# Kernel optimization log

Measured on AMD Instinct MI355X. Metric: run time of the kernel, lower is better.

Reference implementation:

```python
import jax, jax.numpy as jnp
import numpy as np

HID = 5120
H_DEV = 16          # 128 heads / 8 devices
NOPE = 128
ROPE = 64
VDIM = 128
QH = NOPE + ROPE    # 192
Q_LORA = 1536
KV_LORA = 512
EPS = 1e-6
SCALE_DEV = 1.0 / 8.0
ROPE_BASE = 10000.0


def rmsnorm(x, w):
    var = jnp.mean(x * x, axis=-1, keepdims=True)
    return x * jax.lax.rsqrt(var + EPS) * w


def apply_rope(x, pos):
    # DeepSeek-V2: interleaved->blocked reorder, then rotate-half RoPE.
    d = x.shape[-1]
    x = jnp.concatenate([x[..., 0::2], x[..., 1::2]], axis=-1)
    inv = 1.0 / (ROPE_BASE ** (jnp.arange(0, d, 2, dtype=jnp.float32) / d))  # [d/2]
    ang = pos[:, None, :, None].astype(jnp.float32) * inv                     # [b,1,s,d/2]
    cos = jnp.concatenate([jnp.cos(ang), jnp.cos(ang)], axis=-1)
    sin = jnp.concatenate([jnp.sin(ang), jnp.sin(ang)], axis=-1)
    x1, x2 = x[..., : d // 2], x[..., d // 2:]
    return x * cos + jnp.concatenate([-x2, x1], axis=-1) * sin


def setup_inputs() -> dict:
    key = jax.random.key(0)
    ks = jax.random.split(key, 16)
    b, s, past = 1, 2048, 2048
    w = lambda k, shape: (jax.random.normal(k, shape, jnp.float32) * 0.02)
    return {
        "hidden_states": jax.random.normal(ks[0], (b, s, HID), jnp.float32),
        "position_ids": jnp.arange(b * s, dtype=jnp.int32).reshape(b, s),
        "attention_mask": jnp.zeros((b, 1, s, past + s), jnp.float32),
        "past_k": jax.random.normal(ks[1], (b, H_DEV, past, QH), jnp.float32),
        "past_v": jax.random.normal(ks[2], (b, H_DEV, past, VDIM), jnp.float32),
        "w_in_ln": jnp.ones((HID,), jnp.float32),
        "w_qa": w(ks[3], (Q_LORA, HID)),
        "w_qa_ln": jnp.ones((Q_LORA,), jnp.float32),
        "w_qb": w(ks[4], (H_DEV * QH, Q_LORA)),
        "w_kva": w(ks[5], (KV_LORA + ROPE, HID)),
        "w_kva_ln": jnp.ones((KV_LORA,), jnp.float32),
        "w_kvb": w(ks[6], (H_DEV * (NOPE + VDIM), KV_LORA)),
        "w_o": w(ks[7], (HID, H_DEV * VDIM)),
    }


def reference(hidden_states, position_ids, attention_mask, past_k, past_v,
              w_in_ln, w_qa, w_qa_ln, w_qb, w_kva, w_kva_ln, w_kvb, w_o):
    b, s, _ = hidden_states.shape
    residual = hidden_states * SCALE_DEV
    x = rmsnorm(hidden_states, w_in_ln)

    # MLA query: low-rank down, RMSNorm, up to per-device heads
    q = rmsnorm(x @ w_qa.T, w_qa_ln) @ w_qb.T                       # [b,s,H*QH]
    q = q.reshape(b, s, H_DEV, QH).transpose(0, 2, 1, 3)            # [b,H,s,QH]
    q_nope, q_pe = q[..., :NOPE], q[..., NOPE:]

    # MLA key/value: joint compressed kv + shared rope key
    ckv = x @ w_kva.T                                                # [b,s,KV_LORA+ROPE]
    c_kv, k_pe = ckv[..., :KV_LORA], ckv[..., KV_LORA:]
    kv = rmsnorm(c_kv, w_kva_ln) @ w_kvb.T                           # [b,s,H*(NOPE+V)]
    kv = kv.reshape(b, s, H_DEV, NOPE + VDIM).transpose(0, 2, 1, 3)  # [b,H,s,NOPE+V]
    k_nope, v = kv[..., :NOPE], kv[..., NOPE:]
    k_pe = k_pe.reshape(b, 1, s, ROPE)

    q_pe = apply_rope(q_pe, position_ids)
    k_pe = apply_rope(k_pe, position_ids)

    q = jnp.concatenate([q_nope, q_pe], axis=-1)                     # [b,H,s,QH]
    k = jnp.concatenate([k_nope, jnp.broadcast_to(k_pe, (b, H_DEV, s, ROPE))], axis=-1)

    # KV-cache concat -> present kv
    k = jnp.concatenate([past_k, k], axis=2)                         # [b,H,s_kv,QH]
    v = jnp.concatenate([past_v, v], axis=2)                         # [b,H,s_kv,V]

    scores = jnp.einsum('bhqd,bhkd->bhqk', q, k) * (QH ** -0.5) + attention_mask
    attn = jax.nn.softmax(scores, axis=-1)
    ctx = jnp.einsum('bhqk,bhkd->bhqd', attn, v)                     # [b,H,s,V]
    ctx = ctx.transpose(0, 2, 1, 3).reshape(b, s, H_DEV * VDIM)

    out = residual + ctx @ w_o.T
    return out.astype(jnp.float32), k.astype(jnp.float32), v.astype(jnp.float32)
```

## Files before the change

### kernel.cpp

```cpp
#include <hip/hip_runtime.h>
#include <cstdint>

typedef unsigned short ushort_t;
typedef __attribute__((ext_vector_type(8))) short short8;
typedef __attribute__((ext_vector_type(4))) float floatx4;

#define HID    5120
#define NHEAD  16
#define NOPE   128
#define ROPE_D 64
#define VDIM   128
#define QHD    192
#define QLORA  1536
#define KVLORA 512
#define SEQ    2048
#define PAST   2048
#define TOTK   4096
#define NQAKV  2112
#define EPS_RMS 1e-6f
#define SCALE_DEV 0.125f
#define LOG2E 1.4426950408889634f
#define ATT_SCALE 0.07216878364870322f
#define LOG2_10000 13.287712379549449f

__device__ __forceinline__ float bf2f(ushort_t u) {
  unsigned int x = ((unsigned int)u) << 16;
  return __builtin_bit_cast(float, x);
}
__device__ __forceinline__ ushort_t f2bf(float f) {
  unsigned int u = __builtin_bit_cast(unsigned int, f);
  unsigned int r = u + 0x7fffu + ((u >> 16) & 1u);
  return (ushort_t)(r >> 16);
}
__device__ __forceinline__ void unpack8(uint4 c, float* f) {
  const ushort_t* p = (const ushort_t*)&c;
#pragma unroll
  for (int i = 0; i < 8; ++i) f[i] = bf2f(p[i]);
}
__device__ __forceinline__ uint4 pack8(const float* f) {
  uint4 c;
  ushort_t* p = (ushort_t*)&c;
#pragma unroll
  for (int i = 0; i < 8; ++i) p[i] = f2bf(f[i]);
  return c;
}

__global__ void cvt_kernel(const float* __restrict__ src, ushort_t* __restrict__ dst)
{
  long i = ((long)blockIdx.x * 256 + threadIdx.x) * 8;
  float f[8];
  *(float4*)(f)     = *(const float4*)(src + i);
  *(float4*)(f + 4) = *(const float4*)(src + i + 4);
  *(uint4*)(dst + i) = pack8(f);
}

__global__ void zero4_kernel(uint4* __restrict__ dst)
{
  long i = (long)blockIdx.x * 256 + threadIdx.x;
  uint4 z; z.x = 0u; z.y = 0u; z.z = 0u; z.w = 0u;
  dst[i] = z;
}

#define GLDT 40
__global__ __launch_bounds__(256, 2) void gemm_bt(
    const ushort_t* __restrict__ A, const ushort_t* __restrict__ B,
    ushort_t* __restrict__ Cb, float* __restrict__ Cf,
    const float* __restrict__ resid, float resid_scale,
    int M, int N, int K)
{
  __shared__ __align__(16) ushort_t As[128 * GLDT];
  __shared__ __align__(16) ushort_t Bs[128 * GLDT];
  int t = threadIdx.x;
  int lane = t & 63, wave = t >> 6;
  int wm = wave >> 1, wn = wave & 1;
  int lrow = lane & 15, quad = lane >> 4;
  long bm = (long)blockIdx.y * 128;
  long bn = (long)blockIdx.x * 128;

  int r0 = t >> 2, cc = t & 3;
  int r1 = r0 + 64;
  const ushort_t* a0 = A + (bm + r0) * (long)K + cc * 8;
  const ushort_t* a1 = A + (bm + r1) * (long)K + cc * 8;
  long nb0 = bn + r0; if (nb0 > N - 1) nb0 = N - 1;
  long nb1 = bn + r1; if (nb1 > N - 1) nb1 = N - 1;
  const ushort_t* b0 = B + nb0 * (long)K + cc * 8;
  const ushort_t* b1 = B + nb1 * (long)K + cc * 8;

  floatx4 acc[4][4];
#pragma unroll
  for (int i = 0; i < 4; ++i)
#pragma unroll
    for (int j = 0; j < 4; ++j) acc[i][j] = (floatx4)0.f;

  uint4 pa0 = *(const uint4*)a0;
  uint4 pa1 = *(const uint4*)a1;
  uint4 pb0 = *(const uint4*)b0;
  uint4 pb1 = *(const uint4*)b1;

  int nk = K >> 5;
  for (int kt = 0; kt < nk; ++kt) {
    *(uint4*)&As[r0 * GLDT + cc * 8] = pa0;
    *(uint4*)&As[r1 * GLDT + cc * 8] = pa1;
    *(uint4*)&Bs[r0 * GLDT + cc * 8] = pb0;
    *(uint4*)&Bs[r1 * GLDT + cc * 8] = pb1;
    __syncthreads();
    if (kt + 1 < nk) {
      int off = (kt + 1) << 5;
      pa0 = *(const uint4*)(a0 + off);
      pa1 = *(const uint4*)(a1 + off);
      pb0 = *(const uint4*)(b0 + off);
      pb1 = *(const uint4*)(b1 + off);
    }
    short8 af[4], bfr[4];
#pragma unroll
    for (int mt = 0; mt < 4; ++mt)
      af[mt] = *(const short8*)&As[(wm * 64 + mt * 16 + lrow) * GLDT + quad * 8];
#pragma unroll
    for (int nt = 0; nt < 4; ++nt)
      bfr[nt] = *(const short8*)&Bs[(wn * 64 + nt * 16 + lrow) * GLDT + quad * 8];
#pragma unroll
    for (int mt = 0; mt < 4; ++mt)
#pragma unroll
      for (int nt = 0; nt < 4; ++nt)
        acc[mt][nt] = __builtin_amdgcn_mfma_f32_16x16x32_bf16(af[mt], bfr[nt], acc[mt][nt], 0, 0, 0);
    __syncthreads();
  }

#pragma unroll
  for (int mt = 0; mt < 4; ++mt) {
    long grow = bm + wm * 64 + mt * 16 + quad * 4;
#pragma unroll
    for (int nt = 0; nt < 4; ++nt) {
      long gcol = bn + wn * 64 + nt * 16 + lrow;
      if (gcol < N) {
#pragma unroll
        for (int r2 = 0; r2 < 4; ++r2) {
          long row = grow + r2;
          float v = acc[mt][nt][r2];
          if (Cf) {
            if (resid) v += resid_scale * resid[row * (long)N + gcol];
            Cf[row * (long)N + gcol] = v;
          } else {
            Cb[row * (long)N + gcol] = f2bf(v);
          }
        }
      }
    }
  }
}

__global__ __launch_bounds__(256, 2) void gemm_splitk(
    const ushort_t* __restrict__ A, const ushort_t* __restrict__ B,
    float* __restrict__ Cf, int M, int N, int K)
{
  __shared__ __align__(16) ushort_t As[128 * GLDT];
  __shared__ __align__(16) ushort_t Bs[128 * GLDT];
  int t = threadIdx.x;
  int lane = t & 63, wave = t >> 6;
  int wm = wave >> 1, wn = wave & 1;
  int lrow = lane & 15, quad = lane >> 4;
  long bm = (long)blockIdx.y * 128;
  long bn = (long)blockIdx.x * 128;
  int khalf = K >> 1;
  long k0 = (long)blockIdx.z * khalf;

  int r0 = t >> 2, cc = t & 3;
  int r1 = r0 + 64;
  const ushort_t* a0 = A + (bm + r0) * (long)K + k0 + cc * 8;
  const ushort_t* a1 = A + (bm + r1) * (long)K + k0 + cc * 8;
  long nb0 = bn + r0; if (nb0 > N - 1) nb0 = N - 1;
  long nb1 = bn + r1; if (nb1 > N - 1) nb1 = N - 1;
  const ushort_t* b0 = B + nb0 * (long)K + k0 + cc * 8;
  const ushort_t* b1 = B + nb1 * (long)K + k0 + cc * 8;

  floatx4 acc[4][4];
#pragma unroll
  for (int i = 0; i < 4; ++i)
#pragma unroll
    for (int j = 0; j < 4; ++j) acc[i][j] = (floatx4)0.f;

  uint4 pa0 = *(const uint4*)a0;
  uint4 pa1 = *(const uint4*)a1;
  uint4 pb0 = *(const uint4*)b0;
  uint4 pb1 = *(const uint4*)b1;

  int nk = khalf >> 5;
  for (int kt = 0; kt < nk; ++kt) {
    *(uint4*)&As[r0 * GLDT + cc * 8] = pa0;
    *(uint4*)&As[r1 * GLDT + cc * 8] = pa1;
    *(uint4*)&Bs[r0 * GLDT + cc * 8] = pb0;
    *(uint4*)&Bs[r1 * GLDT + cc * 8] = pb1;
    __syncthreads();
    if (kt + 1 < nk) {
      int off = (kt + 1) << 5;
      pa0 = *(const uint4*)(a0 + off);
      pa1 = *(const uint4*)(a1 + off);
      pb0 = *(const uint4*)(b0 + off);
      pb1 = *(const uint4*)(b1 + off);
    }
    short8 af[4], bfr[4];
#pragma unroll
    for (int mt = 0; mt < 4; ++mt)
      af[mt] = *(const short8*)&As[(wm * 64 + mt * 16 + lrow) * GLDT + quad * 8];
#pragma unroll
    for (int nt = 0; nt < 4; ++nt)
      bfr[nt] = *(const short8*)&Bs[(wn * 64 + nt * 16 + lrow) * GLDT + quad * 8];
#pragma unroll
    for (int mt = 0; mt < 4; ++mt)
#pragma unroll
      for (int nt = 0; nt < 4; ++nt)
        acc[mt][nt] = __builtin_amdgcn_mfma_f32_16x16x32_bf16(af[mt], bfr[nt], acc[mt][nt], 0, 0, 0);
    __syncthreads();
  }

#pragma unroll
  for (int mt = 0; mt < 4; ++mt) {
    long grow = bm + wm * 64 + mt * 16 + quad * 4;
#pragma unroll
    for (int nt = 0; nt < 4; ++nt) {
      long gcol = bn + wn * 64 + nt * 16 + lrow;
      if (gcol < N) {
#pragma unroll
        for (int r2 = 0; r2 < 4; ++r2)
          atomicAdd(&Cf[(grow + r2) * (long)N + gcol], acc[mt][nt][r2]);
      }
    }
  }
}

__global__ void rms_in_kernel(const float* __restrict__ x,
                              const float* __restrict__ w,
                              ushort_t* __restrict__ out)
{
  int row = blockIdx.x, t = threadIdx.x;
  const float* xr = x + (long)row * HID + t * 16;
  float v[16];
#pragma unroll
  for (int i = 0; i < 4; ++i) *(float4*)(v + i * 4) = *(const float4*)(xr + i * 4);
  float ss = 0.f;
#pragma unroll
  for (int i = 0; i < 16; ++i) ss += v[i] * v[i];
#pragma unroll
  for (int o = 1; o < 64; o <<= 1) ss += __shfl_xor(ss, o);
  __shared__ float red[5];
  if ((t & 63) == 0) red[t >> 6] = ss;
  __syncthreads();
  float tot = red[0] + red[1] + red[2] + red[3] + red[4];
  float sc = rsqrtf(tot / (float)HID + EPS_RMS);
  float wv[16];
#pragma unroll
  for (int i = 0; i < 4; ++i) *(float4*)(wv + i * 4) = *(const float4*)(w + t * 16 + i * 4);
#pragma unroll
  for (int i = 0; i < 16; ++i) v[i] *= sc * wv[i];
  ushort_t* o = out + (long)row * HID + t * 16;
  *(uint4*)o       = pack8(v);
  *(uint4*)(o + 8) = pack8(v + 8);
}

__global__ void rms_qa_f32(const float* __restrict__ C,
                           const float* __restrict__ w,
                           ushort_t* __restrict__ out)
{
  int row = blockIdx.x, t = threadIdx.x;
  const float* xr = C + (long)row * NQAKV + t * 8;
  float v[8];
  *(float4*)(v)     = *(const float4*)(xr);
  *(float4*)(v + 4) = *(const float4*)(xr + 4);
  float ss = 0.f;
#pragma unroll
  for (int i = 0; i < 8; ++i) ss += v[i] * v[i];
#pragma unroll
  for (int o = 1; o < 64; o <<= 1) ss += __shfl_xor(ss, o);
  __shared__ float red[3];
  if ((t & 63) == 0) red[t >> 6] = ss;
  __syncthreads();
  float tot = red[0] + red[1] + red[2];
  float sc = rsqrtf(tot / (float)QLORA + EPS_RMS);
  float wv[8];
  *(float4*)(wv)     = *(const float4*)(w + t * 8);
  *(float4*)(wv + 4) = *(const float4*)(w + t * 8 + 4);
#pragma unroll
  for (int i = 0; i < 8; ++i) v[i] *= sc * wv[i];
  *(uint4*)(out + (long)row * QLORA + t * 8) = pack8(v);
}

__global__ void rms_ckv_rope_f32(const float* __restrict__ C,
                                 const float* __restrict__ w,
                                 const int* __restrict__ pos_ids,
                                 ushort_t* __restrict__ ckv_n,
                                 ushort_t* __restrict__ kpe,
                                 float* __restrict__ k_out)
{
  int row = blockIdx.x, t = threadIdx.x;
  const float* xr = C + (long)row * NQAKV + QLORA;
  float v[8];
  *(float4*)(v)     = *(const float4*)(xr + t * 8);
  *(float4*)(v + 4) = *(const float4*)(xr + t * 8 + 4);
  float ss = 0.f;
#pragma unroll
  for (int i = 0; i < 8; ++i) ss += v[i] * v[i];
#pragma unroll
  for (int o = 1; o < 64; o <<= 1) ss += __shfl_xor(ss, o);
  float sc = rsqrtf(ss / (float)KVLORA + EPS_RMS);
  float wv[8];
  *(float4*)(wv)     = *(const float4*)(w + t * 8);
  *(float4*)(wv + 4) = *(const float4*)(w + t * 8 + 4);
  float ov[8];
#pragma unroll
  for (int i = 0; i < 8; ++i) ov[i] = v[i] * sc * wv[i];
  *(uint4*)(ckv_n + (long)row * KVLORA + t * 8) = pack8(ov);

  if (t < 32) {
    float e  = xr[512 + 2 * t];
    float od = xr[512 + 2 * t + 1];
    float p = (float)pos_ids[row];
    float inv = __builtin_exp2f(-((float)t / 32.f) * LOG2_10000);
    float ang = p * inv, sn, cs;
    sincosf(ang, &sn, &cs);
    float r1 = e * cs - od * sn;
    float r2 = od * cs + e * sn;
    kpe[(long)row * 64 + t]      = f2bf(r1);
    kpe[(long)row * 64 + 32 + t] = f2bf(r2);
#pragma unroll
    for (int h = 0; h < NHEAD; ++h) {
      float* kr = k_out + ((long)h * TOTK + PAST + row) * QHD + NOPE;
      kr[t] = r1;
      kr[32 + t] = r2;
    }
  }
}

__global__ void qpost_kernel(const ushort_t* __restrict__ q_raw,
                             const int* __restrict__ pos_ids,
                             ushort_t* __restrict__ q_bf)
{
  int row = blockIdx.x, t = threadIdx.x;
  const ushort_t* qr = q_raw + (long)row * 3072;
  ushort_t* qo = q_bf + (long)row * 3072;
  {
    int hh = t >> 4, c = t & 15;
    float v[8];
    unpack8(*(const uint4*)(qr + hh * QHD + c * 8), v);
#pragma unroll
    for (int i = 0; i < 8; ++i) v[i] *= ATT_SCALE;
    *(uint4*)(qo + hh * QHD + c * 8) = pack8(v);
  }
  float p = (float)pos_ids[row];
#pragma unroll
  for (int it = 0; it < 2; ++it) {
    int slot = t + it * 256;
    int hh = slot >> 5, i = slot & 31;
    float e  = bf2f(qr[hh * QHD + NOPE + 2 * i]);
    float od = bf2f(qr[hh * QHD + NOPE + 2 * i + 1]);
    float inv = __builtin_exp2f(-((float)i / 32.f) * LOG2_10000);
    float ang = p * inv, sn, cs;
    sincosf(ang, &sn, &cs);
    qo[hh * QHD + NOPE + i]      = f2bf((e * cs - od * sn) * ATT_SCALE);
    qo[hh * QHD + NOPE + 32 + i] = f2bf((od * cs + e * sn) * ATT_SCALE);
  }
}

__global__ void kvpost_kernel(const ushort_t* __restrict__ kv_raw,
                              float* __restrict__ k_out,
                              float* __restrict__ v_out)
{
  int row = blockIdx.x, t = threadIdx.x;
  const ushort_t* kr = kv_raw + (long)row * 4096;
#pragma unroll
  for (int it = 0; it < 2; ++it) {
    int c = t + it * 256;
    int hh = c >> 5, cc = c & 31;
    float v[8];
    unpack8(*(const uint4*)(kr + c * 8), v);
    float* dst;
    if (cc < 16) dst = k_out + ((long)hh * TOTK + PAST + row) * QHD + cc * 8;
    else         dst = v_out + ((long)hh * TOTK + PAST + row) * VDIM + (cc - 16) * 8;
    floatx4 f0 = {v[0], v[1], v[2], v[3]};
    floatx4 f1 = {v[4], v[5], v[6], v[7]};
    *(floatx4*)dst = f0;
    *(floatx4*)(dst + 4) = f1;
  }
}

__global__ void past_kernel(const float* __restrict__ past_k,
                            const float* __restrict__ past_v,
                            float* __restrict__ k_out,
                            float* __restrict__ v_out)
{
  long c = (long)blockIdx.x * 256 + threadIdx.x;
  if (c < 1572864) {
    float4 v = *(const float4*)(past_k + c * 4);
    long hh = c / 98304, rem = c % 98304;
    long s = rem / 48, cc = rem % 48;
    *(float4*)(k_out + (hh * (long)TOTK + s) * QHD + cc * 4) = v;
  } else {
    long c2 = c - 1572864;
    float4 v = *(const float4*)(past_v + c2 * 4);
    long hh = c2 / 65536, rem = c2 % 65536;
    long s = rem / 32, cc = rem % 32;
    *(float4*)(v_out + (hh * (long)TOTK + s) * VDIM + cc * 4) = v;
  }
}

__global__ void buildK_kernel(const float* __restrict__ past_k,
                              const ushort_t* __restrict__ kv_raw,
                              const ushort_t* __restrict__ kpe,
                              ushort_t* __restrict__ Kc)
{
  long g = (long)blockIdx.x * 256 + threadIdx.x;
  int ko = (int)(g & 63);
  long r = g >> 6;
  int cc = (int)(r % 24);
  long r2 = r / 24;
  int kt = (int)(r2 & 63);
  int hh = (int)(r2 >> 6);
  int key = kt * 64 + ko;
  uint4 val;
  if (key < PAST) {
    const float* src = past_k + ((long)hh * PAST + key) * QHD + cc * 8;
    float f[8];
    *(float4*)(f)     = *(const float4*)src;
    *(float4*)(f + 4) = *(const float4*)(src + 4);
    val = pack8(f);
  } else {
    int s = key - PAST;
    int d0 = cc * 8;
    if (d0 < NOPE) val = *(const uint4*)(kv_raw + (long)s * 4096 + hh * 256 + d0);
    else           val = *(const uint4*)(kpe + (long)s * 64 + (d0 - NOPE));
  }
  *(uint4*)(Kc + g * 8) = val;
}

__global__ void buildV_kernel(const float* __restrict__ past_v,
                              const ushort_t* __restrict__ kv_raw,
                              ushort_t* __restrict__ Vc)
{
  long tid = (long)blockIdx.x * 256 + threadIdx.x;
  int vd = (int)(tid & 127);
  long r = tid >> 7;
  int kchunk = (int)(r & 7);
  long r2 = r >> 3;
  int kt = (int)(r2 & 63);
  int hh = (int)(r2 >> 6);
  int key0 = kt * 64 + kchunk * 8;
  __align__(16) ushort_t tmp[8];
  if (key0 < PAST) {
#pragma unroll
    for (int j = 0; j < 8; ++j)
      tmp[j] = f2bf(past_v[((long)hh * PAST + key0 + j) * VDIM + vd]);
  } else {
    int s = key0 - PAST;
#pragma unroll
    for (int j = 0; j < 8; ++j)
      tmp[j] = kv_raw[(long)(s + j) * 4096 + hh * 256 + NOPE + vd];
  }
  *(uint4*)(Vc + ((((long)hh * 64 + kt) * 128 + vd) * 9 + kchunk) * 8) = *(uint4*)tmp;
}

__global__ __launch_bounds__(256, 3) void attn_kernel(
    const ushort_t* __restrict__ qb,
    const ushort_t* __restrict__ Kc,
    const ushort_t* __restrict__ Vc,
    const float* __restrict__ attn_mask,
    ushort_t* __restrict__ opart,
    float* __restrict__ ml)
{
  __shared__ __align__(16) ushort_t KtL[1536 * 8];
  __shared__ __align__(16) ushort_t VtL[1152 * 8];
  __shared__ __align__(16) ushort_t Pl[4 * 16 * 72];

  int t = threadIdx.x, lane = t & 63, wave = t >> 6;
  int lrow = lane & 15, quad = lane >> 4;
  int lb = blockIdx.x;
  int xcd = lb & 7, j = lb >> 3;
  int h = xcd + 8 * (j / 96);
  int rem = j % 96;
  int sec = rem >> 5;
  int q0 = (rem & 31) * 64;
  int kt_beg = (sec == 0) ? 0 : (sec == 1 ? 22 : 43);
  int kt_end = (sec == 0) ? 22 : (sec == 1 ? 43 : 64);
  int qrow_a = q0 + wave * 16 + lrow;
  int qrow_c = q0 + wave * 16 + quad * 4;

  short8 aq[6];
  const ushort_t* qp = qb + ((long)qrow_a * 16 + h) * QHD + quad * 8;
#pragma unroll
  for (int kc = 0; kc < 6; ++kc) aq[kc] = *(const short8*)(qp + kc * 32);

  float m_r[4], l_r[4];
  floatx4 cacc[8];
#pragma unroll
  for (int r = 0; r < 4; ++r) { m_r[r] = -1e30f; l_r[r] = 0.f; }
#pragma unroll
  for (int v = 0; v < 8; ++v) cacc[v] = (floatx4)0.f;

  const ushort_t* Kbase = Kc + (long)h * 64 * 1536 * 8;
  const ushort_t* Vbase = Vc + (long)h * 64 * 1152 * 8;

  for (int kt2 = kt_beg; kt2 < kt_end; ++kt2) {
    const ushort_t* ks = Kbase + (long)kt2 * 1536 * 8;
#pragma unroll
    for (int i = 0; i < 6; ++i) {
      int s = i * 256 + t;
      *(uint4*)&KtL[s * 8] = *(const uint4*)(ks + (long)s * 8);
    }
    const ushort_t* vs = Vbase + (long)kt2 * 1152 * 8;
#pragma unroll
    for (int i = 0; i < 5; ++i) {
      int s = i * 256 + t;
      if (s < 1152) *(uint4*)&VtL[s * 8] = *(const uint4*)(vs + (long)s * 8);
    }
    __syncthreads();

    floatx4 sacc[4];
#pragma unroll
    for (int nt = 0; nt < 4; ++nt) sacc[nt] = (floatx4)0.f;
    __builtin_amdgcn_s_setprio(1);
#pragma unroll
    for (int kc = 0; kc < 6; ++kc) {
#pragma unroll
      for (int nt = 0; nt < 4; ++nt) {
        short8 bk = *(const short8*)&KtL[(((kc * 4 + quad) * 64) + nt * 16 + lrow) * 8];
        sacc[nt] = __builtin_amdgcn_mfma_f32_16x16x32_bf16(aq[kc], bk, sacc[nt], 0, 0, 0);
      }
    }
    __builtin_amdgcn_s_setprio(0);

    int kbase = kt2 * 64;
    float sv[4][4];
#pragma unroll
    for (int nt = 0; nt < 4; ++nt)
#pragma unroll
      for (int r = 0; r < 4; ++r)
        sv[nt][r] = sacc[nt][r] +
                    attn_mask[(long)(qrow_c + r) * TOTK + kbase + nt * 16 + lrow];

    float mxv[4]; int need = 0;
#pragma unroll
    for (int r = 0; r < 4; ++r) {
      float mx = fmaxf(fmaxf(sv[0][r], sv[1][r]), fmaxf(sv[2][r], sv[3][r]));
      mx = fmaxf(mx, __shfl_xor(mx, 1));
      mx = fmaxf(mx, __shfl_xor(mx, 2));
      mx = fmaxf(mx, __shfl_xor(mx, 4));
      mx = fmaxf(mx, __shfl_xor(mx, 8));
      mxv[r] = mx;
      need |= (mx > m_r[r] + 8.f) ? 1 : 0;
    }
    float alpha[4] = {1.f, 1.f, 1.f, 1.f};
    if (__any(need)) {
#pragma unroll
      for (int r = 0; r < 4; ++r) {
        float mn = fmaxf(m_r[r], mxv[r]);
        alpha[r] = __builtin_exp2f((m_r[r] - mn) * LOG2E);
        m_r[r] = mn;
      }
#pragma unroll
      for (int v = 0; v < 8; ++v) {
        floatx4 c = cacc[v];
        c[0] *= alpha[0]; c[1] *= alpha[1]; c[2] *= alpha[2]; c[3] *= alpha[3];
        cacc[v] = c;
      }
    }
#pragma unroll
    for (int r = 0; r < 4; ++r) {
      float rs = 0.f;
#pragma unroll
      for (int nt = 0; nt < 4; ++nt) {
        float p = __builtin_exp2f((sv[nt][r] - m_r[r]) * LOG2E);
        sv[nt][r] = p;
        rs += p;
      }
      rs += __shfl_xor(rs, 1);
      rs += __shfl_xor(rs, 2);
      rs += __shfl_xor(rs, 4);
      rs += __shfl_xor(rs, 8);
      l_r[r] = l_r[r] * alpha[r] + rs;
    }

    ushort_t* pw = &Pl[wave * 16 * 72];
#pragma unroll
    for (int nt = 0; nt < 4; ++nt)
#pragma unroll
      for (int r = 0; r < 4; ++r)
        pw[(quad * 4 + r) * 72 + nt * 16 + lrow] = f2bf(sv[nt][r]);

    const ushort_t* pr = &Pl[wave * 16 * 72];
    short8 ap[2];
#pragma unroll
    for (int kc = 0; kc < 2; ++kc)
      ap[kc] = *(const short8*)(pr + lrow * 72 + kc * 32 + quad * 8);
    __builtin_amdgcn_s_setprio(1);
#pragma unroll
    for (int kc = 0; kc < 2; ++kc) {
#pragma unroll
      for (int v = 0; v < 8; ++v) {
        short8 bv = *(const short8*)&VtL[(((v * 16 + lrow) * 9) + kc * 4 + quad) * 8];
        cacc[v] = __builtin_amdgcn_mfma_f32_16x16x32_bf16(ap[kc], bv, cacc[v], 0, 0, 0);
      }
    }
    __builtin_amdgcn_s_setprio(0);
    __syncthreads();
  }

  long obase = (long)(sec * 16 + h) * 2048 + qrow_c;
#pragma unroll
  for (int v = 0; v < 8; ++v)
#pragma unroll
    for (int r = 0; r < 4; ++r)
      opart[(obase + r) * 128 + v * 16 + lrow] = f2bf(cacc[v][r]);
  if (lrow == 0) {
#pragma unroll
    for (int r = 0; r < 4; ++r) {
      float* mp = ml + (obase + r) * 2;
      mp[0] = m_r[r];
      mp[1] = l_r[r];
    }
  }
}

__global__ void combine_kernel(const ushort_t* __restrict__ opart,
                               const float* __restrict__ ml,
                               ushort_t* __restrict__ ctx)
{
  int t = threadIdx.x;
  int gr = blockIdx.x * 16 + (t >> 4);
  int h = gr >> 11, qrow = gr & 2047;
  int dc = (t & 15) * 8;
  float m[3], l[3];
#pragma unroll
  for (int s = 0; s < 3; ++s) {
    const float* p = ml + ((long)(s * 16 + h) * 2048 + qrow) * 2;
    m[s] = p[0]; l[s] = p[1];
  }
  float M = fmaxf(fmaxf(m[0], m[1]), m[2]);
  float aa[3], L = 0.f;
#pragma unroll
  for (int s = 0; s < 3; ++s) {
    aa[s] = __builtin_exp2f((m[s] - M) * LOG2E);
    L += aa[s] * l[s];
  }
  float inv = 1.f / L;
  float acc[8] = {0.f, 0.f, 0.f, 0.f, 0.f, 0.f, 0.f, 0.f};
#pragma unroll
  for (int s = 0; s < 3; ++s) {
    uint4 c = *(const uint4*)(opart + ((long)(s * 16 + h) * 2048 + qrow) * 128 + dc);
    float f[8];
    unpack8(c, f);
#pragma unroll
    for (int i = 0; i < 8; ++i) acc[i] += aa[s] * f[i];
  }
  float outv[8];
#pragma unroll
  for (int i = 0; i < 8; ++i) outv[i] = acc[i] * inv;
  *(uint4*)(ctx + (long)qrow * 2048 + h * 128 + dc) = pack8(outv);
}

extern "C" void kernel_launch(void* const* d_in, const int* in_sizes, int n_in,
                              void* d_out, int out_size, void* d_ws, size_t ws_size,
                              hipStream_t stream)
{
  const float* hidden   = (const float*)d_in[0];
  const int*   pos      = (const int*)d_in[1];
  const float* mask     = (const float*)d_in[2];
  const float* past_k   = (const float*)d_in[3];
  const float* past_v   = (const float*)d_in[4];
  const float* w_in_ln  = (const float*)d_in[5];
  const float* w_qa     = (const float*)d_in[6];
  const float* w_qa_ln  = (const float*)d_in[7];
  const float* w_qb     = (const float*)d_in[8];
  const float* w_kva    = (const float*)d_in[9];
  const float* w_kva_ln = (const float*)d_in[10];
  const float* w_kvb    = (const float*)d_in[11];
  const float* w_o      = (const float*)d_in[12];

  float* out0  = (float*)d_out;
  float* k_out = out0 + 10485760;
  float* v_out = k_out + 12582912;

  char* ws = (char*)d_ws;
  ushort_t* x_bf   = (ushort_t*)(ws + 0);
  ushort_t* q_raw  = x_bf;
  ushort_t* kv_raw = x_bf;
  float*    Cqakv  = (float*)(ws + 20971520);
  ushort_t* qa_n   = (ushort_t*)(ws + 38273024);
  ushort_t* q_bf   = (ushort_t*)(ws + 38273024);
  ushort_t* Kc     = (ushort_t*)(ws + 50855936);
  ushort_t* Vc     = (ushort_t*)(ws + 76021760);
  ushort_t* ckv_n  = (ushort_t*)(ws + 94896128);
  ushort_t* kpe    = (ushort_t*)(ws + 96993280);
  ushort_t* ctx    = (ushort_t*)(ws + 94896128);

  ushort_t* opart  = (ushort_t*)(ws + 0);
  float*    mlbuf  = (float*)(ws + 25165824);

  ushort_t* wqakva_bf = Kc;
  ushort_t* wqb_bf    = Vc;
  ushort_t* wkvb_bf   = (ushort_t*)(ws + 76021760 + 9437184);
  ushort_t* wo_bf     = Kc;

  cvt_kernel<<<dim3(3840), dim3(256), 0, stream>>>(w_qa, wqakva_bf);
  cvt_kernel<<<dim3(1440), dim3(256), 0, stream>>>(w_kva, wqakva_bf + 7864320);
  cvt_kernel<<<dim3(2304), dim3(256), 0, stream>>>(w_qb, wqb_bf);
  cvt_kernel<<<dim3(1024), dim3(256), 0, stream>>>(w_kvb, wkvb_bf);

  zero4_kernel<<<dim3(4224), dim3(256), 0, stream>>>((uint4*)Cqakv);

  rms_in_kernel<<<dim3(2048), dim3(320), 0, stream>>>(hidden, w_in_ln, x_bf);

  gemm_splitk<<<dim3(17, 16, 2), dim3(256), 0, stream>>>(x_bf, wqakva_bf, Cqakv,
                                                         2048, NQAKV, 5120);

  rms_qa_f32<<<dim3(2048), dim3(192), 0, stream>>>(Cqakv, w_qa_ln, qa_n);
  rms_ckv_rope_f32<<<dim3(2048), dim3(64), 0, stream>>>(Cqakv, w_kva_ln, pos,
                                                        ckv_n, kpe, k_out);

  gemm_bt<<<dim3(24, 16), dim3(256), 0, stream>>>(qa_n, wqb_bf, q_raw, (float*)nullptr,
                                                  (const float*)nullptr, 0.f, 2048, 3072, 1536);
  qpost_kernel<<<dim3(2048), dim3(256), 0, stream>>>(q_raw, pos, q_bf);

  gemm_bt<<<dim3(32, 16), dim3(256), 0, stream>>>(ckv_n, wkvb_bf, kv_raw, (float*)nullptr,
                                                  (const float*)nullptr, 0.f, 2048, 4096, 512);
  kvpost_kernel<<<dim3(2048), dim3(256), 0, stream>>>(kv_raw, k_out, v_out);
  past_kernel<<<dim3(10240), dim3(256), 0, stream>>>(past_k, past_v, k_out, v_out);

  buildK_kernel<<<dim3(6144), dim3(256), 0, stream>>>(past_k, kv_raw, kpe, Kc);
  buildV_kernel<<<dim3(4096), dim3(256), 0, stream>>>(past_v, kv_raw, Vc);

  attn_kernel<<<dim3(1536), dim3(256), 0, stream>>>(q_bf, Kc, Vc, mask, opart, mlbuf);
  combine_kernel<<<dim3(2048), dim3(256), 0, stream>>>(opart, mlbuf, ctx);

  cvt_kernel<<<dim3(5120), dim3(256), 0, stream>>>(w_o, wo_bf);

  gemm_bt<<<dim3(40, 16), dim3(256), 0, stream>>>(ctx, wo_bf, (ushort_t*)nullptr, out0,
                                                  hidden, SCALE_DEV, 2048, 5120, 2048);
}
```

Baseline: 813.2 us.

## Generalize split-K, apply to q-up and output GEMMs, fuse past_v copy

The split-K GEMM now takes any number of K splits, which become the grid z-dimension. It is used with 3 splits for the qa/kva down-projection, and split-K is extended to the q up-projection (fp32 output into a zeroed buffer) and to the output projection. For the output projection, the residual is pre-written by a separate init kernel and the GEMM accumulates on top of it. The past_v copy into v_out moves into buildV so the past values are read once. The workspace layout is reshuffled to fit the new fp32 buffers. These changes are meant to raise CU occupancy on GEMMs with few tiles and to remove redundant memory traffic, at the cost of atomic accumulation, extra zeroing and init passes, and fp32 intermediates.

```diff
diff --git a/kernel.cpp b/kernel.cpp
--- a/kernel.cpp
+++ b/kernel.cpp
@@ -61,6 +61,15 @@
   dst[i] = z;
 }
 
+__global__ void resid_init_kernel(const float* __restrict__ hidden,
+                                  float* __restrict__ out0)
+{
+  long i = ((long)blockIdx.x * 256 + threadIdx.x) * 4;
+  float4 v = *(const float4*)(hidden + i);
+  v.x *= SCALE_DEV; v.y *= SCALE_DEV; v.z *= SCALE_DEV; v.w *= SCALE_DEV;
+  *(float4*)(out0 + i) = v;
+}
+
 #define GLDT 40
 __global__ __launch_bounds__(256, 2) void gemm_bt(
     const ushort_t* __restrict__ A, const ushort_t* __restrict__ B,
@@ -161,8 +170,13 @@
   int lrow = lane & 15, quad = lane >> 4;
   long bm = (long)blockIdx.y * 128;
   long bn = (long)blockIdx.x * 128;
-  int khalf = K >> 1;
-  long k0 = (long)blockIdx.z * khalf;
+
+  int nkTot = K >> 5;
+  int z = blockIdx.z, nz = gridDim.z;
+  int q = nkTot / nz, rsd = nkTot % nz;
+  int nk = q + (z < rsd ? 1 : 0);
+  int kt0 = z * q + (z < rsd ? z : rsd);
+  long k0 = (long)kt0 << 5;
 
   int r0 = t >> 2, cc = t & 3;
   int r1 = r0 + 64;
@@ -184,7 +198,6 @@
   uint4 pb0 = *(const uint4*)b0;
   uint4 pb1 = *(const uint4*)b1;
 
-  int nk = khalf >> 5;
   for (int kt = 0; kt < nk; ++kt) {
     *(uint4*)&As[r0 * GLDT + cc * 8] = pa0;
     *(uint4*)&As[r1 * GLDT + cc * 8] = pa1;
@@ -330,17 +343,18 @@
   }
 }
 
-__global__ void qpost_kernel(const ushort_t* __restrict__ q_raw,
-                             const int* __restrict__ pos_ids,
-                             ushort_t* __restrict__ q_bf)
+__global__ void qpost_f32(const float* __restrict__ q_raw,
+                          const int* __restrict__ pos_ids,
+                          ushort_t* __restrict__ q_bf)
 {
   int row = blockIdx.x, t = threadIdx.x;
-  const ushort_t* qr = q_raw + (long)row * 3072;
+  const float* qr = q_raw + (long)row * 3072;
   ushort_t* qo = q_bf + (long)row * 3072;
   {
     int hh = t >> 4, c = t & 15;
     float v[8];
-    unpack8(*(const uint4*)(qr + hh * QHD + c * 8), v);
+    *(float4*)(v)     = *(const float4*)(qr + hh * QHD + c * 8);
+    *(float4*)(v + 4) = *(const float4*)(qr + hh * QHD + c * 8 + 4);
 #pragma unroll
     for (int i = 0; i < 8; ++i) v[i] *= ATT_SCALE;
     *(uint4*)(qo + hh * QHD + c * 8) = pack8(v);
@@ -350,8 +364,8 @@
   for (int it = 0; it < 2; ++it) {
     int slot = t + it * 256;
     int hh = slot >> 5, i = slot & 31;
-    float e  = bf2f(qr[hh * QHD + NOPE + 2 * i]);
-    float od = bf2f(qr[hh * QHD + NOPE + 2 * i + 1]);
+    float e  = qr[hh * QHD + NOPE + 2 * i];
+    float od = qr[hh * QHD + NOPE + 2 * i + 1];
     float inv = __builtin_exp2f(-((float)i / 32.f) * LOG2_10000);
     float ang = p * inv, sn, cs;
     sincosf(ang, &sn, &cs);
@@ -383,23 +397,13 @@
 }
 
 __global__ void past_kernel(const float* __restrict__ past_k,
-                            const float* __restrict__ past_v,
-                            float* __restrict__ k_out,
-                            float* __restrict__ v_out)
+                            float* __restrict__ k_out)
 {
   long c = (long)blockIdx.x * 256 + threadIdx.x;
-  if (c < 1572864) {
-    float4 v = *(const float4*)(past_k + c * 4);
-    long hh = c / 98304, rem = c % 98304;
-    long s = rem / 48, cc = rem % 48;
-    *(float4*)(k_out + (hh * (long)TOTK + s) * QHD + cc * 4) = v;
-  } else {
-    long c2 = c - 1572864;
-    float4 v = *(const float4*)(past_v + c2 * 4);
-    long hh = c2 / 65536, rem = c2 % 65536;
-    long s = rem / 32, cc = rem % 32;
-    *(float4*)(v_out + (hh * (long)TOTK + s) * VDIM + cc * 4) = v;
-  }
+  float4 v = *(const float4*)(past_k + c * 4);
+  long hh = c / 98304, rem = c % 98304;
+  long s = rem / 48, cc = rem % 48;
+  *(float4*)(k_out + (hh * (long)TOTK + s) * QHD + cc * 4) = v;
 }
 
 __global__ void buildK_kernel(const float* __restrict__ past_k,
@@ -433,7 +437,8 @@
 
 __global__ void buildV_kernel(const float* __restrict__ past_v,
                               const ushort_t* __restrict__ kv_raw,
-                              ushort_t* __restrict__ Vc)
+                              ushort_t* __restrict__ Vc,
+                              float* __restrict__ v_out)
 {
   long tid = (long)blockIdx.x * 256 + threadIdx.x;
   int vd = (int)(tid & 127);
@@ -446,8 +451,11 @@
   __align__(16) ushort_t tmp[8];
   if (key0 < PAST) {
 #pragma unroll
-    for (int j = 0; j < 8; ++j)
-      tmp[j] = f2bf(past_v[((long)hh * PAST + key0 + j) * VDIM + vd]);
+    for (int j = 0; j < 8; ++j) {
+      float fv = past_v[((long)hh * PAST + key0 + j) * VDIM + vd];
+      v_out[((long)hh * TOTK + key0 + j) * VDIM + vd] = fv;
+      tmp[j] = f2bf(fv);
+    }
   } else {
     int s = key0 - PAST;
 #pragma unroll
@@ -678,25 +686,23 @@
   float* v_out = k_out + 12582912;
 
   char* ws = (char*)d_ws;
-  ushort_t* x_bf   = (ushort_t*)(ws + 0);
-  ushort_t* q_raw  = x_bf;
-  ushort_t* kv_raw = x_bf;
-  float*    Cqakv  = (float*)(ws + 20971520);
-  ushort_t* qa_n   = (ushort_t*)(ws + 38273024);
-  ushort_t* q_bf   = (ushort_t*)(ws + 38273024);
-  ushort_t* Kc     = (ushort_t*)(ws + 50855936);
-  ushort_t* Vc     = (ushort_t*)(ws + 76021760);
-  ushort_t* ckv_n  = (ushort_t*)(ws + 94896128);
-  ushort_t* kpe    = (ushort_t*)(ws + 96993280);
-  ushort_t* ctx    = (ushort_t*)(ws + 94896128);
-
-  ushort_t* opart  = (ushort_t*)(ws + 0);
-  float*    mlbuf  = (float*)(ws + 25165824);
-
-  ushort_t* wqakva_bf = Kc;
-  ushort_t* wqb_bf    = Vc;
-  ushort_t* wkvb_bf   = (ushort_t*)(ws + 76021760 + 9437184);
-  ushort_t* wo_bf     = Kc;
+  ushort_t* wqb_bf    = (ushort_t*)(ws + 0);
+  ushort_t* wkvb_bf   = (ushort_t*)(ws + 9437184);
+  ushort_t* qa_n      = (ushort_t*)(ws + 13631488);
+  ushort_t* q_bf      = (ushort_t*)(ws + 13631488);
+  ushort_t* kpe       = (ushort_t*)(ws + 26214400);
+  ushort_t* ckv_n     = (ushort_t*)(ws + 26476544);
+  ushort_t* wqakva_bf = (ushort_t*)(ws + 28573696);
+  float*    Cq3       = (float*)   (ws + 28573696);
+  ushort_t* Vc        = (ushort_t*)(ws + 28573696);
+  ushort_t* ctx       = (ushort_t*)(ws + 28573696);
+  ushort_t* x_bf      = (ushort_t*)(ws + 53739520);
+  ushort_t* Kc        = (ushort_t*)(ws + 53739520);
+  ushort_t* wo_bf     = (ushort_t*)(ws + 53739520);
+  float*    Cqakv     = (float*)   (ws + 78905344);
+  ushort_t* kv_raw    = (ushort_t*)(ws + 78905344);
+  ushort_t* opart     = (ushort_t*)(ws + 78905344);
+  float*    mlbuf     = (float*)   (ws + 104071168);
 
   cvt_kernel<<<dim3(3840), dim3(256), 0, stream>>>(w_qa, wqakva_bf);
   cvt_kernel<<<dim3(1440), dim3(256), 0, stream>>>(w_kva, wqakva_bf + 7864320);
@@ -704,33 +710,33 @@
   cvt_kernel<<<dim3(1024), dim3(256), 0, stream>>>(w_kvb, wkvb_bf);
 
   zero4_kernel<<<dim3(4224), dim3(256), 0, stream>>>((uint4*)Cqakv);
-
   rms_in_kernel<<<dim3(2048), dim3(320), 0, stream>>>(hidden, w_in_ln, x_bf);
 
-  gemm_splitk<<<dim3(17, 16, 2), dim3(256), 0, stream>>>(x_bf, wqakva_bf, Cqakv,
+  gemm_splitk<<<dim3(17, 16, 3), dim3(256), 0, stream>>>(x_bf, wqakva_bf, Cqakv,
                                                          2048, NQAKV, 5120);
 
   rms_qa_f32<<<dim3(2048), dim3(192), 0, stream>>>(Cqakv, w_qa_ln, qa_n);
   rms_ckv_rope_f32<<<dim3(2048), dim3(64), 0, stream>>>(Cqakv, w_kva_ln, pos,
                                                         ckv_n, kpe, k_out);
 
-  gemm_bt<<<dim3(24, 16), dim3(256), 0, stream>>>(qa_n, wqb_bf, q_raw, (float*)nullptr,
-                                                  (const float*)nullptr, 0.f, 2048, 3072, 1536);
-  qpost_kernel<<<dim3(2048), dim3(256), 0, stream>>>(q_raw, pos, q_bf);
+  zero4_kernel<<<dim3(6144), dim3(256), 0, stream>>>((uint4*)Cq3);
+  gemm_splitk<<<dim3(24, 16, 2), dim3(256), 0, stream>>>(qa_n, wqb_bf, Cq3,
+                                                         2048, 3072, 1536);
+  qpost_f32<<<dim3(2048), dim3(256), 0, stream>>>(Cq3, pos, q_bf);
 
   gemm_bt<<<dim3(32, 16), dim3(256), 0, stream>>>(ckv_n, wkvb_bf, kv_raw, (float*)nullptr,
                                                   (const float*)nullptr, 0.f, 2048, 4096, 512);
   kvpost_kernel<<<dim3(2048), dim3(256), 0, stream>>>(kv_raw, k_out, v_out);
-  past_kernel<<<dim3(10240), dim3(256), 0, stream>>>(past_k, past_v, k_out, v_out);
+  past_kernel<<<dim3(6144), dim3(256), 0, stream>>>(past_k, k_out);
 
   buildK_kernel<<<dim3(6144), dim3(256), 0, stream>>>(past_k, kv_raw, kpe, Kc);
-  buildV_kernel<<<dim3(4096), dim3(256), 0, stream>>>(past_v, kv_raw, Vc);
+  buildV_kernel<<<dim3(4096), dim3(256), 0, stream>>>(past_v, kv_raw, Vc, v_out);
 
   attn_kernel<<<dim3(1536), dim3(256), 0, stream>>>(q_bf, Kc, Vc, mask, opart, mlbuf);
   combine_kernel<<<dim3(2048), dim3(256), 0, stream>>>(opart, mlbuf, ctx);
 
   cvt_kernel<<<dim3(5120), dim3(256), 0, stream>>>(w_o, wo_bf);
-
-  gemm_bt<<<dim3(40, 16), dim3(256), 0, stream>>>(ctx, wo_bf, (ushort_t*)nullptr, out0,
-                                                  hidden, SCALE_DEV, 2048, 5120, 2048);
-}
+  resid_init_kernel<<<dim3(10240), dim3(256), 0, stream>>>(hidden, out0);
+  gemm_splitk<<<dim3(40, 16, 2), dim3(256), 0, stream>>>(ctx, wo_bf, out0,
+                                                         2048, 5120, 2048);
+}
```

Measured after the change: 854.6 us. +5.1%, slower.
